# Kernel tuning notes

Hardware: AMD Instinct MI355X
Metric: run time of the kernel (lower is better)

Reference implementation:

```python
import jax, jax.numpy as jnp
import numpy as np

EPS = 1e-5

def _ln(x, g, b):
    mu = jnp.mean(x, axis=-1, keepdims=True)
    var = jnp.mean(jnp.square(x - mu), axis=-1, keepdims=True)
    return (x - mu) * jax.lax.rsqrt(var + EPS) * g + b

def _lrelu(x):
    return jnp.where(x >= 0, x, 0.1 * x)  # LeakyReLU(0.1)

def _layer(x, w, b, g, be, act):
    # PointLinearLayer: Linear -> LayerNorm -> (optional) LeakyReLU(0.1)
    y = _ln(jnp.matmul(x, w) + b, g, be)
    return _lrelu(y) if act else y

def setup_inputs():
    key = jax.random.key(0)
    ks = jax.random.split(key, 16)
    B, Ns, Nd, K, Cin, Cout, PE, M = 1, 10000, 40000, 16, 128, 128, 32, 16
    w = lambda k, i, o: jax.random.normal(k, (i, o), jnp.float32) * 0.02
    z = lambda n: jnp.zeros((n,), jnp.float32)
    o = lambda n: jnp.ones((n,), jnp.float32)
    return {
        "sparse_xyz": jax.random.normal(ks[0], (B, Ns, 3), jnp.float32),
        "sparse_feats": jax.random.normal(ks[1], (B, Ns, Cin), jnp.float32),
        "nei_inds": jax.random.randint(ks[2], (B, Nd, K), 0, Ns),
        "sparse_xyz_norm": jax.random.normal(ks[3], (B, Ns, 3), jnp.float32),
        "dense_xyz": jax.random.normal(ks[4], (B, Nd, 3), jnp.float32),
        "dense_xyz_norm": jax.random.normal(ks[5], (B, Nd, 3), jnp.float32),
        "dense_feats": jax.random.normal(ks[6], (B, Nd, Cout), jnp.float32),
        # pe_convs WeightNet(3 -> 32, hidden=[32]): L0 3->32 LN+act, L1 32->32 LN
        "pe_w0": w(ks[7], 3, PE), "pe_b0": z(PE), "pe_g0": o(PE), "pe_be0": z(PE),
        "pe_w1": w(ks[8], PE, PE), "pe_b1": z(PE), "pe_g1": o(PE), "pe_be1": z(PE),
        # main WeightNet(3 -> 16, hidden=[16,16]): L0,L1 LN+act, L2 LN
        "wn_w0": w(ks[9], 3, M), "wn_b0": z(M), "wn_g0": o(M), "wn_be0": z(M),
        "wn_w1": w(ks[10], M, M), "wn_b1": z(M), "wn_g1": o(M), "wn_be1": z(M),
        "wn_w2": w(ks[11], M, M), "wn_b2": z(M), "wn_g2": o(M), "wn_be2": z(M),
        # final PointLinearLayer: (Cin+PE)*M -> Cout with LN + LeakyReLU(0.1)
        "lin_w": w(ks[12], (Cin + PE) * M, Cout), "lin_b": z(Cout),
        "lin_g": o(Cout), "lin_be": z(Cout),
    }

def reference(sparse_xyz, sparse_feats, nei_inds, sparse_xyz_norm, dense_xyz,
              dense_xyz_norm, dense_feats,
              pe_w0, pe_b0, pe_g0, pe_be0, pe_w1, pe_b1, pe_g1, pe_be1,
              wn_w0, wn_b0, wn_g0, wn_be0, wn_w1, wn_b1, wn_g1, wn_be1,
              wn_w2, wn_b2, wn_g2, wn_be2, lin_w, lin_b, lin_g, lin_be):
    gather = jax.vmap(lambda t, i: t[i])  # per-batch kNN gather
    loc = gather(sparse_xyz, nei_inds) - dense_xyz[:, :, None, :]   # B,Nd,K,3 relative coords (weightNetInput, USE_VI=False)
    g_feat = gather(sparse_feats, nei_inds)                          # B,Nd,K,Cin
    # positional-encoding WeightNet on relative coords (USE_PE)
    pe = _layer(loc, pe_w0, pe_b0, pe_g0, pe_be0, True)
    pe = _layer(pe, pe_w1, pe_b1, pe_g1, pe_be1, False)              # B,Nd,K,32
    feat = jnp.concatenate([g_feat, pe], axis=-1)                    # B,Nd,K,Cin+32
    # main WeightNet generates per-neighbor mixing weights
    wts = _layer(loc, wn_w0, wn_b0, wn_g0, wn_be0, True)
    wts = _layer(wts, wn_w1, wn_b1, wn_g1, wn_be1, True)
    wts = _layer(wts, wn_w2, wn_b2, wn_g2, wn_be2, False)            # B,Nd,K,16
    B, Nd = nei_inds.shape[:2]
    # matmul(feat^T, wts) over K, flatten channel x mid dims (C-major, matches torch .view)
    out = jnp.einsum('bnkc,bnkm->bncm', feat, wts).reshape(B, Nd, -1)
    out = _layer(out, lin_w, lin_b, lin_g, lin_be, True)             # B,Nd,Cout
    return out + dense_feats                                         # shortcut dense features
```

## Files before the change

kernel.cpp:

```cpp
#include <hip/hip_runtime.h>

#define NPB  16
#define KNN  16
#define CIN  128
#define CF   160
#define MM   16
#define PEC  32
#define COUT 128
#define KDIM 2560
#define LEPS 1e-5f

typedef __bf16 bf16x8 __attribute__((ext_vector_type(8)));
typedef float  f32x4  __attribute__((ext_vector_type(4)));
union U16x8 { uint4 u4; bf16x8 b; unsigned short us[8]; };

#define SW_PE_W0   0
#define SW_PE_B0   96
#define SW_PE_G0   128
#define SW_PE_BE0  160
#define SW_PE_W1   192
#define SW_PE_B1   1216
#define SW_PE_G1   1248
#define SW_PE_BE1  1280
#define SW_WN_W0   1312
#define SW_WN_B0   1360
#define SW_WN_G0   1376
#define SW_WN_BE0  1392
#define SW_WN_W1   1408
#define SW_WN_B1   1664
#define SW_WN_G1   1680
#define SW_WN_BE1  1696
#define SW_WN_W2   1712
#define SW_WN_B2   1968
#define SW_WN_G2   1984
#define SW_WN_BE2  2000
#define SW_TOTAL   2016

__device__ __forceinline__ float bf2f(unsigned short b){
  union { unsigned int u; float f; } x; x.u = ((unsigned int)b) << 16; return x.f;
}
__device__ __forceinline__ unsigned short f2bf(float f){
  union { float f; unsigned int u; } x; x.f = f;
  unsigned int r = (x.u + 0x7fffu + ((x.u >> 16) & 1u)) >> 16;
  return (unsigned short)r;
}
__device__ __forceinline__ unsigned short f2b(float f){
  union { __bf16 h; unsigned short u; } v; v.h = (__bf16)f; return v.u;
}
__device__ __forceinline__ float rsum16(float v){
  v += __shfl_xor(v, 8, 16);
  v += __shfl_xor(v, 4, 16);
  v += __shfl_xor(v, 2, 16);
  v += __shfl_xor(v, 1, 16);
  return v;
}
__device__ __forceinline__ float rsum8(float v){
  v += __shfl_xor(v, 4, 8);
  v += __shfl_xor(v, 2, 8);
  v += __shfl_xor(v, 1, 8);
  return v;
}
__device__ __forceinline__ float rsum32(float v){
  v += __shfl_xor(v, 16, 32);
  v += __shfl_xor(v, 8, 32);
  v += __shfl_xor(v, 4, 32);
  v += __shfl_xor(v, 2, 32);
  v += __shfl_xor(v, 1, 32);
  return v;
}
__device__ __forceinline__ float lrelu(float v){ return v >= 0.f ? v : 0.1f * v; }

template<int N>
__device__ __forceinline__ void ln_inlane(float* v, const float* g, const float* be, bool act){
  float mu = 0.f;
#pragma unroll
  for (int i = 0; i < N; ++i) mu += v[i];
  mu *= (1.f / N);
  float var = 0.f;
#pragma unroll
  for (int i = 0; i < N; ++i) { float d = v[i] - mu; var += d * d; }
  const float rs = rsqrtf(var * (1.f / N) + LEPS);
#pragma unroll
  for (int i = 0; i < N; ++i) {
    float y = (v[i] - mu) * rs * g[i] + be[i];
    v[i] = act ? lrelu(y) : y;
  }
}

__global__ __launch_bounds__(256)
void pct_prep(const float* __restrict__ lin_w, unsigned short* __restrict__ wpack,
              const float* __restrict__ sf, unsigned short* __restrict__ sfb16,
              const int n4)
{
  const int bid = blockIdx.x;
  if (bid < 160) {
    const int u    = bid * 256 + threadIdx.x;
    const int lane = u & 63;
    const int tt   = (u >> 6) & 7;
    const int s    = u >> 9;
    const int ipb  = s * 32 + ((lane >> 4) * 8);
    const int nn   = tt * 16 + (lane & 15);
    unsigned short v[8];
#pragma unroll
    for (int j = 0; j < 8; ++j) {
      const int ip  = ipb + j;
      const int r   = ip & 3;
      const int ctl = (ip >> 2) & 1;
      const int qq  = (ip >> 3) & 3;
      const int c16 = (ip >> 5) & 15;
      const int P   = ip >> 9;
      const int c   = P * 32 + ctl * 16 + c16;
      const int m   = qq * 4 + r;
      v[j] = f2bf(lin_w[(long)(c * MM + m) * COUT + nn]);
    }
    *(uint4*)(wpack + (long)u * 8) = *(uint4*)v;
  } else {
    const int i = (bid - 160) * 256 + threadIdx.x;
    if (i >= n4) return;
    const float4 v = ((const float4*)sf)[i];
    union { unsigned short us[4]; uint2 u; } r;
    r.us[0] = f2b(v.x); r.us[1] = f2b(v.y); r.us[2] = f2b(v.z); r.us[3] = f2b(v.w);
    ((uint2*)sfb16)[i] = r.u;
  }
}

__global__ __launch_bounds__(256)
void pct_nets(
    const float* __restrict__ sparse_xyz,
    const int* __restrict__ nei_inds,
    const float* __restrict__ dense_xyz,
    const float* __restrict__ pe_w0, const float* __restrict__ pe_b0,
    const float* __restrict__ pe_g0, const float* __restrict__ pe_be0,
    const float* __restrict__ pe_w1, const float* __restrict__ pe_b1,
    const float* __restrict__ pe_g1, const float* __restrict__ pe_be1,
    const float* __restrict__ wn_w0, const float* __restrict__ wn_b0,
    const float* __restrict__ wn_g0, const float* __restrict__ wn_be0,
    const float* __restrict__ wn_w1, const float* __restrict__ wn_b1,
    const float* __restrict__ wn_g1, const float* __restrict__ wn_be1,
    const float* __restrict__ wn_w2, const float* __restrict__ wn_b2,
    const float* __restrict__ wn_g2, const float* __restrict__ wn_be2,
    unsigned short* __restrict__ apack)
{
  __shared__ float sw[SW_TOTAL];
  __shared__ __align__(16) unsigned short wtsf[16 * 256];
  __shared__ __align__(16) unsigned short pef[16 * 512];

  const int t     = threadIdx.x;
  const int nbase = blockIdx.x * NPB;

  for (int i = t; i < 96;   i += 256) sw[SW_PE_W0 + i] = pe_w0[i];
  for (int i = t; i < 32;   i += 256) {
    sw[SW_PE_B0 + i] = pe_b0[i];  sw[SW_PE_G0 + i] = pe_g0[i];  sw[SW_PE_BE0 + i] = pe_be0[i];
    sw[SW_PE_B1 + i] = pe_b1[i];  sw[SW_PE_G1 + i] = pe_g1[i];  sw[SW_PE_BE1 + i] = pe_be1[i];
  }
  for (int i = t; i < 1024; i += 256) sw[SW_PE_W1 + i] = pe_w1[i];
  for (int i = t; i < 48;   i += 256) sw[SW_WN_W0 + i] = wn_w0[i];
  for (int i = t; i < 16;   i += 256) {
    sw[SW_WN_B0 + i] = wn_b0[i];  sw[SW_WN_G0 + i] = wn_g0[i];  sw[SW_WN_BE0 + i] = wn_be0[i];
    sw[SW_WN_B1 + i] = wn_b1[i];  sw[SW_WN_G1 + i] = wn_g1[i];  sw[SW_WN_BE1 + i] = wn_be1[i];
    sw[SW_WN_B2 + i] = wn_b2[i];  sw[SW_WN_G2 + i] = wn_g2[i];  sw[SW_WN_BE2 + i] = wn_be2[i];
  }
  for (int i = t; i < 256;  i += 256) { sw[SW_WN_W1 + i] = wn_w1[i]; sw[SW_WN_W2 + i] = wn_w2[i]; }
  __syncthreads();

  {
    const int p  = t >> 4;
    const int kk = t & 15;
    const int n  = nbase + p;
    const int idx = nei_inds[n * KNN + kk];
    const float x0 = sparse_xyz[idx*3+0] - dense_xyz[n*3+0];
    const float x1 = sparse_xyz[idx*3+1] - dense_xyz[n*3+1];
    const float x2 = sparse_xyz[idx*3+2] - dense_xyz[n*3+2];

    float h[32];
#pragma unroll
    for (int c = 0; c < 32; ++c)
      h[c] = x0*sw[SW_PE_W0+c] + x1*sw[SW_PE_W0+32+c] + x2*sw[SW_PE_W0+64+c] + sw[SW_PE_B0+c];
    ln_inlane<32>(h, &sw[SW_PE_G0], &sw[SW_PE_BE0], true);

    float z[32];
#pragma unroll
    for (int c = 0; c < 32; ++c) z[c] = sw[SW_PE_B1 + c];
#pragma unroll 4
    for (int j = 0; j < 32; ++j) {
      const float hj = h[j];
#pragma unroll
      for (int c = 0; c < 32; ++c) z[c] += hj * sw[SW_PE_W1 + j*32 + c];
    }
    ln_inlane<32>(z, &sw[SW_PE_G1], &sw[SW_PE_BE1], false);
    {
      union { unsigned short us[32]; uint4 u4[4]; } zb;
#pragma unroll
      for (int c = 0; c < 32; ++c) zb.us[c] = f2b(z[c]);
      unsigned short* pp_ = pef + p*512 + kk*32;
#pragma unroll
      for (int j = 0; j < 4; ++j) *(uint4*)(pp_ + j*8) = zb.u4[j];
    }

    float w[16];
#pragma unroll
    for (int m = 0; m < 16; ++m)
      w[m] = x0*sw[SW_WN_W0+m] + x1*sw[SW_WN_W0+16+m] + x2*sw[SW_WN_W0+32+m] + sw[SW_WN_B0+m];
    ln_inlane<16>(w, &sw[SW_WN_G0], &sw[SW_WN_BE0], true);

    float z2[16];
#pragma unroll
    for (int m = 0; m < 16; ++m) z2[m] = sw[SW_WN_B1 + m];
#pragma unroll 4
    for (int j = 0; j < 16; ++j) {
      const float wj = w[j];
#pragma unroll
      for (int m = 0; m < 16; ++m) z2[m] += wj * sw[SW_WN_W1 + j*16 + m];
    }
    ln_inlane<16>(z2, &sw[SW_WN_G1], &sw[SW_WN_BE1], true);

#pragma unroll
    for (int m = 0; m < 16; ++m) w[m] = sw[SW_WN_B2 + m];
#pragma unroll 4
    for (int j = 0; j < 16; ++j) {
      const float wj = z2[j];
#pragma unroll
      for (int m = 0; m < 16; ++m) w[m] += wj * sw[SW_WN_W2 + j*16 + m];
    }
    ln_inlane<16>(w, &sw[SW_WN_G2], &sw[SW_WN_BE2], false);
    {
      unsigned short* wf = wtsf + p*256 + ((kk >> 3) << 7) + (kk & 7);
#pragma unroll
      for (int m = 0; m < 16; ++m) wf[m*8] = f2b(w[m]);
    }
  }

  {
    const int lane = t & 63;
    const int wave = t >> 6;
    const int l2   = lane & 31;
    const int ct2  = lane >> 5;
#pragma unroll
    for (int i = 0; i < 4; ++i) {
      const int p = wave*4 + i;
      unsigned short* fw = apack + (size_t)(nbase + p) * KDIM;
      if (lane < 32) {
        const uint4 a = *(const uint4*)(wtsf + p*256 + lane*8);
        *(uint4*)(fw + lane*8) = a;
      }
      union { unsigned short us[8]; uint4 u4; } o;
#pragma unroll
      for (int j = 0; j < 8; ++j)
        o.us[j] = pef[p*512 + ((l2 >> 4)*8 + j)*32 + ct2*16 + (l2 & 15)];
      *(uint4*)(fw + 256 + ct2*256 + l2*8) = o.u4;
    }
  }
}

__global__ __launch_bounds__(256, 4)
void pct_einsum2(
    const int* __restrict__ nei_inds,
    const unsigned short* __restrict__ sfb16,
    unsigned short* __restrict__ apack)
{
  __shared__ __align__(16) char stage[4 * 2 * 4096];

  const int t     = threadIdx.x;
  const int nbase = blockIdx.x * NPB;
  const int lane  = t & 63;
  const int wave  = t >> 6;
  const int q     = lane >> 4;
  const int mq    = lane & 15;
  char* stw = stage + wave * 8192;

  int idxall[4][4];
#pragma unroll
  for (int i = 0; i < 4; ++i)
#pragma unroll
    for (int t4 = 0; t4 < 4; ++t4)
      idxall[i][t4] = nei_inds[(nbase + wave*4 + i) * KNN + t4*4 + q];

  U16x8 af[2], pe0[2], pe1[2];
  const uint4 zero4 = {0u, 0u, 0u, 0u};

#define LOADF(i_, b_) do {                                                     \
    const unsigned short* fw_ = apack + (size_t)(nbase + wave*4 + (i_)) * KDIM; \
    af[b_].u4  = (lane < 32) ? *(const uint4*)(fw_ + lane*8) : zero4;          \
    pe0[b_].u4 = *(const uint4*)(fw_ + 256 + (lane & 31)*8);                   \
    pe1[b_].u4 = *(const uint4*)(fw_ + 512 + (lane & 31)*8);                   \
  } while (0)

#define GLDS(i_, b_) do {                                                     \
    _Pragma("unroll")                                                         \
    for (int t4 = 0; t4 < 4; ++t4)                                            \
      __builtin_amdgcn_global_load_lds(                                       \
          (const void*)(sfb16 + (size_t)idxall[i_][t4] * CIN + mq * 8),       \
          (void*)(stw + (b_) * 4096 + t4 * 1024), 16, 0, 0);                  \
  } while (0)

  LOADF(0, 0);
  GLDS(0, 0);

  f32x4 accs[10];
#pragma unroll
  for (int i = 0; i < 4; ++i) {
    const size_t n = (size_t)(nbase + wave*4 + i);

    __builtin_amdgcn_sched_barrier(0);
    if (i < 3) { LOADF(i+1, (i+1)&1); GLDS(i+1, (i+1)&1); }
    if (i == 0)      asm volatile("s_waitcnt vmcnt(7)"  ::: "memory");
    else if (i == 3) asm volatile("s_waitcnt vmcnt(5)"  ::: "memory");
    else             asm volatile("s_waitcnt vmcnt(12)" ::: "memory");
    __builtin_amdgcn_sched_barrier(0);

#pragma unroll
    for (int ct = 0; ct < 10; ++ct) accs[ct] = (f32x4){0.f, 0.f, 0.f, 0.f};

    const unsigned short* sb = (const unsigned short*)(stw + (i & 1) * 4096)
                               + (q & 1) * 1024 + mq;
#pragma unroll
    for (int ct = 0; ct < 8; ++ct) {
      U16x8 bf_;
#pragma unroll
      for (int j = 0; j < 8; ++j) bf_.us[j] = sb[j * CIN + ct * 16];
      accs[ct] = __builtin_amdgcn_mfma_f32_16x16x32_bf16(af[i&1].b, bf_.b, accs[ct], 0, 0, 0);
    }
    accs[8] = __builtin_amdgcn_mfma_f32_16x16x32_bf16(af[i&1].b, pe0[i&1].b, accs[8], 0, 0, 0);
    accs[9] = __builtin_amdgcn_mfma_f32_16x16x32_bf16(af[i&1].b, pe1[i&1].b, accs[9], 0, 0, 0);

    unsigned short* ap = apack + n * KDIM + mq * 32 + q * 8;
#pragma unroll
    for (int P = 0; P < 5; ++P) {
      union { unsigned short us[8]; uint4 u4; } o;
#pragma unroll
      for (int r = 0; r < 4; ++r) {
        o.us[r]     = f2b(accs[2*P    ][r]);
        o.us[4 + r] = f2b(accs[2*P + 1][r]);
      }
      *(uint4*)(ap + P * 512) = o.u4;
    }
  }
#undef LOADF
#undef GLDS
}

__global__ __launch_bounds__(256)
void pct_gemm32(
    const unsigned short* __restrict__ apack,
    const unsigned short* __restrict__ wpack,
    const float* __restrict__ lin_b, const float* __restrict__ lin_g,
    const float* __restrict__ lin_be, const float* __restrict__ dense_feats,
    float* __restrict__ out)
{
  __shared__ __align__(16) union ShU {
    char  abuf[4][2][4096];
    float outs[32][132];
  } sh;

  const int t    = threadIdx.x;
  const int lane = t & 63;
  const int wave = t >> 6;
  const int n0   = blockIdx.x * 32;

  const int q      = lane >> 4;
  const int mq     = lane & 15;
  const int r0     = (wave & 1) * 16;
  const int ttbase = (wave >> 1) * 4;

  char* wb = sh.abuf[wave][0];

  f32x4 acc0 = {0.f,0.f,0.f,0.f}, acc1 = {0.f,0.f,0.f,0.f};
  f32x4 acc2 = {0.f,0.f,0.f,0.f}, acc3 = {0.f,0.f,0.f,0.f};

#define STAGEC(c_, b_) do {                                                   \
    _Pragma("unroll")                                                         \
    for (int a_ = 0; a_ < 4; ++a_) {                                          \
      const int lr_ = 4*a_ + q;                                               \
      const unsigned short* src_ = apack + (size_t)(n0 + r0 + lr_) * KDIM     \
                                 + (c_)*128 + ((mq ^ (lr_ & 7)) * 8);         \
      __builtin_amdgcn_global_load_lds((const void*)src_,                     \
          (void*)(wb + (b_)*4096 + a_*1024), 16, 0, 0);                       \
    }                                                                         \
  } while (0)

#define CHUNK(c_, b_) do {                                                    \
    _Pragma("unroll")                                                         \
    for (int s_ = 0; s_ < 4; ++s_) {                                          \
      const int sg_ = (c_)*4 + s_;                                            \
      U16x8 afr_;                                                             \
      const unsigned short* ar_ = (const unsigned short*)(wb + (b_)*4096)     \
          + mq*128 + (((s_*4 + q) ^ (mq & 7)) * 8);                           \
      afr_.u4 = *(const uint4*)ar_;                                           \
      const unsigned short* wpb_ = wpack + (size_t)sg_*4096 + ttbase*512 + lane*8; \
      U16x8 b0_, b1_, b2_, b3_;                                               \
      b0_.u4 = *(const uint4*)(wpb_);                                         \
      b1_.u4 = *(const uint4*)(wpb_ + 512);                                   \
      b2_.u4 = *(const uint4*)(wpb_ + 1024);                                  \
      b3_.u4 = *(const uint4*)(wpb_ + 1536);                                  \
      acc0 = __builtin_amdgcn_mfma_f32_16x16x32_bf16(afr_.b, b0_.b, acc0, 0,0,0); \
      acc1 = __builtin_amdgcn_mfma_f32_16x16x32_bf16(afr_.b, b1_.b, acc1, 0,0,0); \
      acc2 = __builtin_amdgcn_mfma_f32_16x16x32_bf16(afr_.b, b2_.b, acc2, 0,0,0); \
      acc3 = __builtin_amdgcn_mfma_f32_16x16x32_bf16(afr_.b, b3_.b, acc3, 0,0,0); \
    }                                                                         \
  } while (0)

  STAGEC(0, 0);
#pragma unroll 1
  for (int c = 0; c < 19; ++c) {
    STAGEC(c+1, (c+1)&1);
    asm volatile("s_waitcnt vmcnt(4)" ::: "memory");
    __builtin_amdgcn_sched_barrier(0);
    CHUNK(c, c & 1);
  }
  asm volatile("s_waitcnt vmcnt(0)" ::: "memory");
  __builtin_amdgcn_sched_barrier(0);
  CHUNK(19, 1);
#undef STAGEC
#undef CHUNK

  __syncthreads();

  {
#pragma unroll
    for (int r = 0; r < 4; ++r) {
      sh.outs[r0 + q*4 + r][(ttbase+0)*16 + mq] = acc0[r];
      sh.outs[r0 + q*4 + r][(ttbase+1)*16 + mq] = acc1[r];
      sh.outs[r0 + q*4 + r][(ttbase+2)*16 + mq] = acc2[r];
      sh.outs[r0 + q*4 + r][(ttbase+3)*16 + mq] = acc3[r];
    }
  }
  __syncthreads();

  {
    const int p  = t >> 3;
    const int l8 = t & 7;
    const int n  = n0 + p;
    float v[16];
#pragma unroll
    for (int i = 0; i < 4; ++i) {
      const int cb = (i*8 + l8) * 4;
      const float4 r  = *(const float4*)(&sh.outs[p][cb]);
      const float4 bb = *(const float4*)(lin_b + cb);
      v[i*4+0] = r.x + bb.x; v[i*4+1] = r.y + bb.y;
      v[i*4+2] = r.z + bb.z; v[i*4+3] = r.w + bb.w;
    }
    float sum = 0.f;
#pragma unroll
    for (int i = 0; i < 16; ++i) sum += v[i];
    const float mu = rsum8(sum) * (1.f/128.f);
    float qs = 0.f;
#pragma unroll
    for (int i = 0; i < 16; ++i) { float d = v[i] - mu; qs += d*d; }
    const float rs = rsqrtf(rsum8(qs) * (1.f/128.f) + LEPS);
#pragma unroll
    for (int i = 0; i < 4; ++i) {
      const int cb = (i*8 + l8) * 4;
      const float4 g  = *(const float4*)(lin_g  + cb);
      const float4 be = *(const float4*)(lin_be + cb);
      const float4 df = *(const float4*)(dense_feats + (long)n*COUT + cb);
      float4 y;
      y.x = lrelu((v[i*4+0]-mu)*rs*g.x + be.x) + df.x;
      y.y = lrelu((v[i*4+1]-mu)*rs*g.y + be.y) + df.y;
      y.z = lrelu((v[i*4+2]-mu)*rs*g.z + be.z) + df.z;
      y.w = lrelu((v[i*4+3]-mu)*rs*g.w + be.w) + df.w;
      *(float4*)(out + (long)n*COUT + cb) = y;
    }
  }
}

__global__ __launch_bounds__(256)
void pct_fused(
    const float* __restrict__ sparse_xyz,
    const float* __restrict__ sparse_feats,
    const int* __restrict__ nei_inds,
    const float* __restrict__ dense_xyz,
    const float* __restrict__ dense_feats,
    const float* __restrict__ pe_w0, const float* __restrict__ pe_b0,
    const float* __restrict__ pe_g0, const float* __restrict__ pe_be0,
    const float* __restrict__ pe_w1, const float* __restrict__ pe_b1,
    const float* __restrict__ pe_g1, const float* __restrict__ pe_be1,
    const float* __restrict__ wn_w0, const float* __restrict__ wn_b0,
    const float* __restrict__ wn_g0, const float* __restrict__ wn_be0,
    const float* __restrict__ wn_w1, const float* __restrict__ wn_b1,
    const float* __restrict__ wn_g1, const float* __restrict__ wn_be1,
    const float* __restrict__ wn_w2, const float* __restrict__ wn_b2,
    const float* __restrict__ wn_g2, const float* __restrict__ wn_be2,
    const float* __restrict__ lin_w, const float* __restrict__ lin_b,
    const float* __restrict__ lin_g, const float* __restrict__ lin_be,
    float* __restrict__ out)
{
  __shared__ __align__(16) unsigned short feat_s[KNN][CF];
  __shared__ float wts_s[KNN][MM];
  __shared__ float loc_s[KNN][3];
  __shared__ int   nei_s[KNN];
  __shared__ __align__(16) unsigned short out_tile[CF*MM][8];

  const int t  = threadIdx.x;
  const int n0 = blockIdx.x * 8;
  const int k  = t >> 4;
  const int l  = t & 15;

#pragma unroll 1
  for (int p = 0; p < 8; ++p) {
    const int n = n0 + p;
    if (t < KNN) {
      int idx = nei_inds[n*KNN + t];
      nei_s[t] = idx;
      loc_s[t][0] = sparse_xyz[idx*3+0] - dense_xyz[n*3+0];
      loc_s[t][1] = sparse_xyz[idx*3+1] - dense_xyz[n*3+1];
      loc_s[t][2] = sparse_xyz[idx*3+2] - dense_xyz[n*3+2];
    }
    __syncthreads();
    {
      const int gk = t >> 4;
      const int c8 = (t & 15) * 8;
      const float* src = sparse_feats + (long)nei_s[gk]*CIN + c8;
      const float4 va = *(const float4*)(src);
      const float4 vb = *(const float4*)(src + 4);
      unsigned short* dst = &feat_s[gk][c8];
      dst[0] = f2bf(va.x); dst[1] = f2bf(va.y); dst[2] = f2bf(va.z); dst[3] = f2bf(va.w);
      dst[4] = f2bf(vb.x); dst[5] = f2bf(vb.y); dst[6] = f2bf(vb.z); dst[7] = f2bf(vb.w);
    }
    const float x0 = loc_s[k][0], x1 = loc_s[k][1], x2 = loc_s[k][2];
    const int c0 = l, c1 = l + 16;
    float ha = x0*pe_w0[0*PEC+c0] + x1*pe_w0[1*PEC+c0] + x2*pe_w0[2*PEC+c0] + pe_b0[c0];
    float hb = x0*pe_w0[0*PEC+c1] + x1*pe_w0[1*PEC+c1] + x2*pe_w0[2*PEC+c1] + pe_b0[c1];
    {
      float mu = rsum16(ha + hb) * (1.f/32.f);
      float da = ha - mu, db = hb - mu;
      float q  = rsum16(da*da + db*db);
      float rs = rsqrtf(q*(1.f/32.f) + LEPS);
      ha = lrelu(da*rs*pe_g0[c0] + pe_be0[c0]);
      hb = lrelu(db*rs*pe_g0[c1] + pe_be0[c1]);
    }
    float za = pe_b1[c0], zb = pe_b1[c1];
#pragma unroll
    for (int j = 0; j < 16; ++j) {
      float va = __shfl(ha, j, 16);
      float vb = __shfl(hb, j, 16);
      za += va * pe_w1[j*PEC + c0] + vb * pe_w1[(j+16)*PEC + c0];
      zb += va * pe_w1[j*PEC + c1] + vb * pe_w1[(j+16)*PEC + c1];
    }
    {
      float mu = rsum16(za + zb) * (1.f/32.f);
      float da = za - mu, db = zb - mu;
      float q  = rsum16(da*da + db*db);
      float rs = rsqrtf(q*(1.f/32.f) + LEPS);
      feat_s[k][CIN + c0] = f2bf(da*rs*pe_g1[c0] + pe_be1[c0]);
      feat_s[k][CIN + c1] = f2bf(db*rs*pe_g1[c1] + pe_be1[c1]);
    }
    float w0v = x0*wn_w0[0*MM+l] + x1*wn_w0[1*MM+l] + x2*wn_w0[2*MM+l] + wn_b0[l];
    {
      float mu = rsum16(w0v) * (1.f/16.f);
      float d  = w0v - mu;
      float rs = rsqrtf(rsum16(d*d)*(1.f/16.f) + LEPS);
      w0v = lrelu(d*rs*wn_g0[l] + wn_be0[l]);
    }
    float w1v = wn_b1[l];
#pragma unroll
    for (int j = 0; j < 16; ++j)
      w1v += __shfl(w0v, j, 16) * wn_w1[j*MM + l];
    {
      float mu = rsum16(w1v) * (1.f/16.f);
      float d  = w1v - mu;
      float rs = rsqrtf(rsum16(d*d)*(1.f/16.f) + LEPS);
      w1v = lrelu(d*rs*wn_g1[l] + wn_be1[l]);
    }
    float w2v = wn_b2[l];
#pragma unroll
    for (int j = 0; j < 16; ++j)
      w2v += __shfl(w1v, j, 16) * wn_w2[j*MM + l];
    {
      float mu = rsum16(w2v) * (1.f/16.f);
      float d  = w2v - mu;
      float rs = rsqrtf(rsum16(d*d)*(1.f/16.f) + LEPS);
      w2v = d*rs*wn_g2[l] + wn_be2[l];
    }
    wts_s[k][l] = w2v;
    __syncthreads();
    {
      const int m = t & 15;
      const int g = t >> 4;
      float wv[KNN];
#pragma unroll
      for (int kk = 0; kk < KNN; ++kk) wv[kk] = wts_s[kk][m];
#pragma unroll
      for (int j = 0; j < 10; ++j) {
        const int c = g*10 + j;
        float acc = 0.f;
#pragma unroll
        for (int kk = 0; kk < KNN; ++kk)
          acc += bf2f(feat_s[kk][c]) * wv[kk];
        out_tile[c*MM + m][p] = f2bf(acc);
      }
    }
    __syncthreads();
  }
  {
    const int h  = t >> 6;
    const int o0 = (t & 63) * 2;
    float acc0[8], acc1[8];
#pragma unroll
    for (int p = 0; p < 8; ++p) { acc0[p] = 0.f; acc1[p] = 0.f; }
    const int i0 = h * 640;
    for (int i = i0; i < i0 + 640; ++i) {
      const float2 wv = *(const float2*)(lin_w + (long)i*COUT + o0);
      const float wa = wv.x;
      const float wc = wv.y;
      const uint4 r = *(const uint4*)(&out_tile[i][0]);
      const float f0 = bf2f((unsigned short)(r.x & 0xffffu));
      const float f1 = bf2f((unsigned short)(r.x >> 16));
      const float g2 = bf2f((unsigned short)(r.y & 0xffffu));
      const float g3 = bf2f((unsigned short)(r.y >> 16));
      const float g4 = bf2f((unsigned short)(r.z & 0xffffu));
      const float g5 = bf2f((unsigned short)(r.z >> 16));
      const float g6 = bf2f((unsigned short)(r.w & 0xffffu));
      const float g7 = bf2f((unsigned short)(r.w >> 16));
      acc0[0] += f0*wa; acc1[0] += f0*wc;
      acc0[1] += f1*wa; acc1[1] += f1*wc;
      acc0[2] += g2*wa; acc1[2] += g2*wc;
      acc0[3] += g3*wa; acc1[3] += g3*wc;
      acc0[4] += g4*wa; acc1[4] += g4*wc;
      acc0[5] += g5*wa; acc1[5] += g5*wc;
      acc0[6] += g6*wa; acc1[6] += g6*wc;
      acc0[7] += g7*wa; acc1[7] += g7*wc;
    }
    __syncthreads();
    float* red = (float*)&out_tile[0][0];
#pragma unroll
    for (int p = 0; p < 8; ++p) {
      red[((h*8 + p) << 7) + o0    ] = acc0[p];
      red[((h*8 + p) << 7) + o0 + 1] = acc1[p];
    }
    __syncthreads();
    const int p2 = t >> 5, l2 = t & 31;
    const int n  = n0 + p2;
    float v[4];
#pragma unroll
    for (int j = 0; j < 4; ++j) {
      const int o = l2 + (j << 5);
      float sv = red[((0*8 + p2) << 7) + o] + red[((1*8 + p2) << 7) + o]
               + red[((2*8 + p2) << 7) + o] + red[((3*8 + p2) << 7) + o];
      v[j] = sv + lin_b[o];
    }
    float mu = rsum32(v[0] + v[1] + v[2] + v[3]) * (1.f/128.f);
    float q = 0.f;
#pragma unroll
    for (int j = 0; j < 4; ++j) { float d = v[j] - mu; q += d*d; }
    float rs = rsqrtf(rsum32(q) * (1.f/128.f) + LEPS);
#pragma unroll
    for (int j = 0; j < 4; ++j) {
      const int o = l2 + (j << 5);
      float y = (v[j] - mu) * rs * lin_g[o] + lin_be[o];
      y = lrelu(y);
      y += dense_feats[n*COUT + o];
      out[n*COUT + o] = y;
    }
  }
}

extern "C" void kernel_launch(void* const* d_in, const int* in_sizes, int n_in,
                              void* d_out, int out_size, void* d_ws, size_t ws_size,
                              hipStream_t stream) {
  const int Nd = in_sizes[2] / KNN;
  const int Ns = in_sizes[1] / CIN;
  const size_t a_bytes  = (size_t)Nd * KDIM * 2;
  const size_t w_bytes  = (size_t)KDIM * COUT * 2;
  const size_t f_bytes  = (size_t)Ns * CIN * 2;
  const bool use_split = (ws_size >= a_bytes + w_bytes + f_bytes)
                         && (Nd % 32 == 0) && ((Ns * CIN) % 4 == 0);

  if (use_split) {
    unsigned short* apack = (unsigned short*)d_ws;
    unsigned short* wpack = (unsigned short*)((char*)d_ws + a_bytes);
    unsigned short* sfb16 = (unsigned short*)((char*)d_ws + a_bytes + w_bytes);

    const int n4 = Ns * CIN / 4;
    pct_prep<<<dim3(160 + (n4 + 255)/256), dim3(256), 0, stream>>>(
      (const float*)d_in[27], wpack, (const float*)d_in[1], sfb16, n4);

    pct_nets<<<dim3(Nd / NPB), dim3(256), 0, stream>>>(
      (const float*)d_in[0],  (const int*)d_in[2],  (const float*)d_in[4],
      (const float*)d_in[7],  (const float*)d_in[8],  (const float*)d_in[9],  (const float*)d_in[10],
      (const float*)d_in[11], (const float*)d_in[12], (const float*)d_in[13], (const float*)d_in[14],
      (const float*)d_in[15], (const float*)d_in[16], (const float*)d_in[17], (const float*)d_in[18],
      (const float*)d_in[19], (const float*)d_in[20], (const float*)d_in[21], (const float*)d_in[22],
      (const float*)d_in[23], (const float*)d_in[24], (const float*)d_in[25], (const float*)d_in[26],
      apack);

    pct_einsum2<<<dim3(Nd / NPB), dim3(256), 0, stream>>>(
      (const int*)d_in[2], sfb16, apack);

    pct_gemm32<<<dim3(Nd / 32), dim3(256), 0, stream>>>(
      apack, wpack,
      (const float*)d_in[28], (const float*)d_in[29], (const float*)d_in[30],
      (const float*)d_in[6], (float*)d_out);
  } else {
    pct_fused<<<dim3(Nd / 8), dim3(256), 0, stream>>>(
      (const float*)d_in[0],  (const float*)d_in[1],  (const int*)d_in[2],
      (const float*)d_in[4],  (const float*)d_in[6],
      (const float*)d_in[7],  (const float*)d_in[8],  (const float*)d_in[9],  (const float*)d_in[10],
      (const float*)d_in[11], (const float*)d_in[12], (const float*)d_in[13], (const float*)d_in[14],
      (const float*)d_in[15], (const float*)d_in[16], (const float*)d_in[17], (const float*)d_in[18],
      (const float*)d_in[19], (const float*)d_in[20], (const float*)d_in[21], (const float*)d_in[22],
      (const float*)d_in[23], (const float*)d_in[24], (const float*)d_in[25], (const float*)d_in[26],
      (const float*)d_in[27], (const float*)d_in[28], (const float*)d_in[29], (const float*)d_in[30],
      (float*)d_out);
  }
}
```

Before: 328.1 us.

## Widen final GEMM tile to 64 rows with shared A staging across waves

After: 321.3 us. -2.1%, faster.

```diff
diff --git a/kernel.cpp b/kernel.cpp
--- a/kernel.cpp
+++ b/kernel.cpp
@@ -54,10 +54,9 @@
   v += __shfl_xor(v, 1, 16);
   return v;
 }
-__device__ __forceinline__ float rsum8(float v){
-  v += __shfl_xor(v, 4, 8);
-  v += __shfl_xor(v, 2, 8);
-  v += __shfl_xor(v, 1, 8);
+__device__ __forceinline__ float rsum4(float v){
+  v += __shfl_xor(v, 2, 4);
+  v += __shfl_xor(v, 1, 4);
   return v;
 }
 __device__ __forceinline__ float rsum32(float v){
@@ -340,7 +339,7 @@
 }
 
 __global__ __launch_bounds__(256)
-void pct_gemm32(
+void pct_gemm64(
     const unsigned short* __restrict__ apack,
     const unsigned short* __restrict__ wpack,
     const float* __restrict__ lin_b, const float* __restrict__ lin_g,
@@ -348,92 +347,94 @@
     float* __restrict__ out)
 {
   __shared__ __align__(16) union ShU {
-    char  abuf[4][2][4096];
-    float outs[32][132];
+    char  abuf[2][16384];
+    float outs[64][132];
   } sh;
 
   const int t    = threadIdx.x;
   const int lane = t & 63;
   const int wave = t >> 6;
-  const int n0   = blockIdx.x * 32;
-
-  const int q      = lane >> 4;
-  const int mq     = lane & 15;
-  const int r0     = (wave & 1) * 16;
-  const int ttbase = (wave >> 1) * 4;
-
-  char* wb = sh.abuf[wave][0];
-
-  f32x4 acc0 = {0.f,0.f,0.f,0.f}, acc1 = {0.f,0.f,0.f,0.f};
-  f32x4 acc2 = {0.f,0.f,0.f,0.f}, acc3 = {0.f,0.f,0.f,0.f};
-
-#define STAGEC(c_, b_) do {                                                   \
+  const int n0   = blockIdx.x * 64;
+  const int q    = lane >> 4;
+  const int mq   = lane & 15;
+
+  const unsigned short* wp0 = wpack + ((size_t)(wave*2) * 64 + lane) * 8;
+
+  f32x4 acc[4][2];
+#pragma unroll
+  for (int i = 0; i < 4; ++i)
+#pragma unroll
+    for (int j = 0; j < 2; ++j) acc[i][j] = (f32x4){0.f,0.f,0.f,0.f};
+
+#define STAGE64(c_, b_) do {                                                  \
     _Pragma("unroll")                                                         \
     for (int a_ = 0; a_ < 4; ++a_) {                                          \
-      const int lr_ = 4*a_ + q;                                               \
-      const unsigned short* src_ = apack + (size_t)(n0 + r0 + lr_) * KDIM     \
-                                 + (c_)*128 + ((mq ^ (lr_ & 7)) * 8);         \
-      __builtin_amdgcn_global_load_lds((const void*)src_,                     \
-          (void*)(wb + (b_)*4096 + a_*1024), 16, 0, 0);                       \
+      const int r_ = a_*16 + wave*4 + q;                                      \
+      const unsigned short* s_ = apack + (size_t)(n0 + r_) * KDIM             \
+                               + (c_)*128 + ((mq ^ (r_ & 7)) * 8);            \
+      __builtin_amdgcn_global_load_lds((const void*)s_,                       \
+          (void*)(sh.abuf[b_] + a_*4096 + wave*1024), 16, 0, 2);              \
     }                                                                         \
   } while (0)
 
-#define CHUNK(c_, b_) do {                                                    \
+#define CHUNK64(c_, b_) do {                                                  \
     _Pragma("unroll")                                                         \
     for (int s_ = 0; s_ < 4; ++s_) {                                          \
       const int sg_ = (c_)*4 + s_;                                            \
-      U16x8 afr_;                                                             \
-      const unsigned short* ar_ = (const unsigned short*)(wb + (b_)*4096)     \
-          + mq*128 + (((s_*4 + q) ^ (mq & 7)) * 8);                           \
-      afr_.u4 = *(const uint4*)ar_;                                           \
-      const unsigned short* wpb_ = wpack + (size_t)sg_*4096 + ttbase*512 + lane*8; \
-      U16x8 b0_, b1_, b2_, b3_;                                               \
+      const unsigned short* wpb_ = wp0 + (size_t)sg_ * 4096;                  \
+      U16x8 b0_, b1_;                                                         \
       b0_.u4 = *(const uint4*)(wpb_);                                         \
       b1_.u4 = *(const uint4*)(wpb_ + 512);                                   \
-      b2_.u4 = *(const uint4*)(wpb_ + 1024);                                  \
-      b3_.u4 = *(const uint4*)(wpb_ + 1536);                                  \
-      acc0 = __builtin_amdgcn_mfma_f32_16x16x32_bf16(afr_.b, b0_.b, acc0, 0,0,0); \
-      acc1 = __builtin_amdgcn_mfma_f32_16x16x32_bf16(afr_.b, b1_.b, acc1, 0,0,0); \
-      acc2 = __builtin_amdgcn_mfma_f32_16x16x32_bf16(afr_.b, b2_.b, acc2, 0,0,0); \
-      acc3 = __builtin_amdgcn_mfma_f32_16x16x32_bf16(afr_.b, b3_.b, acc3, 0,0,0); \
+      _Pragma("unroll")                                                       \
+      for (int i_ = 0; i_ < 4; ++i_) {                                        \
+        U16x8 af_;                                                            \
+        const char* ar_ = sh.abuf[b_] + (i_*16 + mq)*256                      \
+                        + (((s_*4 + q) ^ (mq & 7)) * 16);                     \
+        af_.u4 = *(const uint4*)ar_;                                          \
+        acc[i_][0] = __builtin_amdgcn_mfma_f32_16x16x32_bf16(af_.b, b0_.b, acc[i_][0], 0,0,0); \
+        acc[i_][1] = __builtin_amdgcn_mfma_f32_16x16x32_bf16(af_.b, b1_.b, acc[i_][1], 0,0,0); \
+      }                                                                       \
     }                                                                         \
   } while (0)
 
-  STAGEC(0, 0);
+  STAGE64(0, 0);
 #pragma unroll 1
   for (int c = 0; c < 19; ++c) {
-    STAGEC(c+1, (c+1)&1);
+    STAGE64(c+1, (c+1) & 1);
     asm volatile("s_waitcnt vmcnt(4)" ::: "memory");
+    __builtin_amdgcn_s_barrier();
     __builtin_amdgcn_sched_barrier(0);
-    CHUNK(c, c & 1);
+    CHUNK64(c, c & 1);
+    __builtin_amdgcn_s_barrier();
   }
   asm volatile("s_waitcnt vmcnt(0)" ::: "memory");
+  __builtin_amdgcn_s_barrier();
   __builtin_amdgcn_sched_barrier(0);
-  CHUNK(19, 1);
-#undef STAGEC
-#undef CHUNK
+  CHUNK64(19, 1);
+#undef STAGE64
+#undef CHUNK64
 
   __syncthreads();
 
   {
 #pragma unroll
-    for (int r = 0; r < 4; ++r) {
-      sh.outs[r0 + q*4 + r][(ttbase+0)*16 + mq] = acc0[r];
-      sh.outs[r0 + q*4 + r][(ttbase+1)*16 + mq] = acc1[r];
-      sh.outs[r0 + q*4 + r][(ttbase+2)*16 + mq] = acc2[r];
-      sh.outs[r0 + q*4 + r][(ttbase+3)*16 + mq] = acc3[r];
-    }
+    for (int i = 0; i < 4; ++i)
+#pragma unroll
+      for (int j = 0; j < 2; ++j)
+#pragma unroll
+        for (int r = 0; r < 4; ++r)
+          sh.outs[i*16 + q*4 + r][(wave*2 + j)*16 + mq] = acc[i][j][r];
   }
   __syncthreads();
 
   {
-    const int p  = t >> 3;
-    const int l8 = t & 7;
+    const int p  = t >> 2;
+    const int l4 = t & 3;
     const int n  = n0 + p;
-    float v[16];
-#pragma unroll
-    for (int i = 0; i < 4; ++i) {
-      const int cb = (i*8 + l8) * 4;
+    float v[32];
+#pragma unroll
+    for (int i = 0; i < 8; ++i) {
+      const int cb = (i*4 + l4) * 4;
       const float4 r  = *(const float4*)(&sh.outs[p][cb]);
       const float4 bb = *(const float4*)(lin_b + cb);
       v[i*4+0] = r.x + bb.x; v[i*4+1] = r.y + bb.y;
@@ -441,15 +442,15 @@
     }
     float sum = 0.f;
 #pragma unroll
-    for (int i = 0; i < 16; ++i) sum += v[i];
-    const float mu = rsum8(sum) * (1.f/128.f);
+    for (int i = 0; i < 32; ++i) sum += v[i];
+    const float mu = rsum4(sum) * (1.f/128.f);
     float qs = 0.f;
 #pragma unroll
-    for (int i = 0; i < 16; ++i) { float d = v[i] - mu; qs += d*d; }
-    const float rs = rsqrtf(rsum8(qs) * (1.f/128.f) + LEPS);
-#pragma unroll
-    for (int i = 0; i < 4; ++i) {
-      const int cb = (i*8 + l8) * 4;
+    for (int i = 0; i < 32; ++i) { float d = v[i] - mu; qs += d*d; }
+    const float rs = rsqrtf(rsum4(qs) * (1.f/128.f) + LEPS);
+#pragma unroll
+    for (int i = 0; i < 8; ++i) {
+      const int cb = (i*4 + l4) * 4;
       const float4 g  = *(const float4*)(lin_g  + cb);
       const float4 be = *(const float4*)(lin_be + cb);
       const float4 df = *(const float4*)(dense_feats + (long)n*COUT + cb);
@@ -663,7 +664,7 @@
   const size_t w_bytes  = (size_t)KDIM * COUT * 2;
   const size_t f_bytes  = (size_t)Ns * CIN * 2;
   const bool use_split = (ws_size >= a_bytes + w_bytes + f_bytes)
-                         && (Nd % 32 == 0) && ((Ns * CIN) % 4 == 0);
+                         && (Nd % 64 == 0) && ((Ns * CIN) % 4 == 0);
 
   if (use_split) {
     unsigned short* apack = (unsigned short*)d_ws;
@@ -686,7 +687,7 @@
     pct_einsum2<<<dim3(Nd / NPB), dim3(256), 0, stream>>>(
       (const int*)d_in[2], sfb16, apack);
 
-    pct_gemm32<<<dim3(Nd / 32), dim3(256), 0, stream>>>(
+    pct_gemm64<<<dim3(Nd / 64), dim3(256), 0, stream>>>(
       apack, wpack,
       (const float*)d_in[28], (const float*)d_in[29], (const float*)d_in[30],
       (const float*)d_in[6], (float*)d_out);
```
